# Performance work log

Hardware: AMD Instinct MI355X
Metric: run time of the kernel (lower is better)

Reference implementation:

```python
import jax, jax.numpy as jnp
import numpy as np

OUT_SIZE = 7          # output_size
RATIO = 2             # sampling_ratio
STRIDES = (4, 8, 16, 32)  # feature_map_strides, levels P2..P5
CANONICAL = 224.0


def _bilinear_sample(fm, ys, xs):
    """fm: [H,W,C]; ys: [R,K]; xs: [R,K] -> [R,K,K,C] samples at (y[r,ky], x[r,kx]).
    Out-of-range points (y<=-1 or y>=H, same for x) produce 0, matching ROIAlign."""
    H, W, C = fm.shape
    vy = (ys > -1.0) & (ys < H)
    vx = (xs > -1.0) & (xs < W)
    y = jnp.clip(ys, 0.0, H - 1.0)
    x = jnp.clip(xs, 0.0, W - 1.0)
    y0 = jnp.floor(y).astype(jnp.int32)
    x0 = jnp.floor(x).astype(jnp.int32)
    y1 = jnp.minimum(y0 + 1, H - 1)
    x1 = jnp.minimum(x0 + 1, W - 1)
    ly = y - y0; hy = 1.0 - ly  # [R,K]
    lx = x - x0; hx = 1.0 - lx
    f00 = fm[y0[:, :, None], x0[:, None, :]]  # [R,Ky,Kx,C]
    f01 = fm[y0[:, :, None], x1[:, None, :]]
    f10 = fm[y1[:, :, None], x0[:, None, :]]
    f11 = fm[y1[:, :, None], x1[:, None, :]]
    w00 = (hy[:, :, None] * hx[:, None, :])[..., None]
    w01 = (hy[:, :, None] * lx[:, None, :])[..., None]
    w10 = (ly[:, :, None] * hx[:, None, :])[..., None]
    w11 = (ly[:, :, None] * lx[:, None, :])[..., None]
    val = w00 * f00 + w01 * f01 + w10 * f10 + w11 * f11
    mask = (vy[:, :, None] & vx[:, None, :])[..., None]
    return jnp.where(mask, val, 0.0)


def _roi_align_one(fm, boxes):
    """fm: [H,W,C]; boxes: [R,4] in this feature map's coords -> [R,C,S,S]."""
    x1, y1, x2, y2 = boxes[:, 0], boxes[:, 1], boxes[:, 2], boxes[:, 3]
    rw = jnp.maximum(x2 - x1, 1.0)
    rh = jnp.maximum(y2 - y1, 1.0)
    S, r = OUT_SIZE, RATIO
    K = S * r
    g = (jnp.arange(K, dtype=jnp.float32) + 0.5) / r  # sample grid in bin units
    ys = y1[:, None] + g[None, :] * (rh / S)[:, None]  # [R,K]
    xs = x1[:, None] + g[None, :] * (rw / S)[:, None]
    v = _bilinear_sample(fm, ys, xs)                   # [R,K,K,C]
    R_ = v.shape[0]; C = fm.shape[-1]
    v = v.reshape(R_, S, r, S, r, C).mean(axis=(2, 4))  # avg over sampling points
    return v.transpose(0, 3, 1, 2)                      # [R,C,S,S]


def setup_inputs() -> dict:
    key = jax.random.key(0)
    ks = jax.random.split(key, 5)
    B, C, N = 4, 256, 512
    fm2 = jax.random.normal(ks[0], (B, 256, 256, C), dtype=jnp.float32)
    fm3 = jax.random.normal(ks[1], (B, 128, 128, C), dtype=jnp.float32)
    fm4 = jax.random.normal(ks[2], (B, 64, 64, C), dtype=jnp.float32)
    fm5 = jax.random.normal(ks[3], (B, 32, 32, C), dtype=jnp.float32)
    pts = jax.random.uniform(ks[4], (B, N, 2, 2), minval=0.0, maxval=1024.0)
    lo = jnp.min(pts, axis=2)  # [B,N,2] -> (x1,y1)
    hi = jnp.max(pts, axis=2)  # [B,N,2] -> (x2,y2)
    rois = jnp.concatenate([lo, hi], axis=-1)  # [B,N,4]
    return {"fm2": fm2, "fm3": fm3, "fm4": fm4, "fm5": fm5, "rois": rois}


def reference(fm2, fm3, fm4, fm5, rois):
    # FPN level assignment (image coords)
    x1, y1, x2, y2 = rois[..., 0], rois[..., 1], rois[..., 2], rois[..., 3]
    area = (y2 - y1) * (x2 - x1)
    lvl = jnp.log(jnp.sqrt(area) / CANONICAL) / jnp.log(2.0) + 4.0
    lvl = jnp.clip(jnp.round(lvl).astype(jnp.int32), 2, 5)  # [B,N]

    out = 0.0
    for i, (fm, stride) in enumerate(zip((fm2, fm3, fm4, fm5), STRIDES)):
        scale = 1.0 / stride
        aligned = jax.vmap(lambda f, b: _roi_align_one(f, b * scale))(fm, rois)
        out = out + jnp.where((lvl == i + 2)[:, :, None, None, None], aligned, 0.0)
    return out  # [B,N,C,S,S]
```

## Files before the change

kernel.cpp:

```cpp
#include <hip/hip_runtime.h>


constexpr int S     = 7;
constexpr int SS    = 49;
constexpr int CCH   = 256;
constexpr int NROI  = 512;
constexpr int BATCH = 4;
constexpr int CPAD  = 260;

__global__ __launch_bounds__(512, 4) void roialign_kernel(
    const float* __restrict__ fm2, const float* __restrict__ fm3,
    const float* __restrict__ fm4, const float* __restrict__ fm5,
    const float* __restrict__ rois, float* __restrict__ out)
{
    __shared__ float    tile[SS * CPAD];
    __shared__ float    s_wyh[14], s_wyl[14], s_wxh[14], s_wxl[14];
    __shared__ unsigned s_ry0[14], s_ry1[14], s_cx0[14], s_cx1[14];

    const int roi = blockIdx.x;
    const int b   = roi >> 9;

    const float x1  = rois[roi * 4 + 0];
    const float y1v = rois[roi * 4 + 1];
    const float x2  = rois[roi * 4 + 2];
    const float y2v = rois[roi * 4 + 3];

    const float area = (y2v - y1v) * (x2 - x1);
    const float lraw = logf(sqrtf(area) * (1.0f / 224.0f)) * 1.4426950408889634f + 4.0f;
    int lvl = (int)rintf(lraw);
    lvl = lvl < 2 ? 2 : (lvl > 5 ? 5 : lvl);

    const float* fm; int H; float scale;
    if (lvl == 2)      { fm = fm2; H = 256; scale = 0.25f;    }
    else if (lvl == 3) { fm = fm3; H = 128; scale = 0.125f;   }
    else if (lvl == 4) { fm = fm4; H = 64;  scale = 0.0625f;  }
    else               { fm = fm5; H = 32;  scale = 0.03125f; }
    const int W = H;
    fm += (size_t)b * H * W * CCH;

    const float bx1 = x1 * scale, by1 = y1v * scale;
    const float rw  = fmaxf(x2 * scale - bx1, 1.0f);
    const float rh  = fmaxf(y2v * scale - by1, 1.0f);
    const float stx = rw * (1.0f / 7.0f);
    const float sty = rh * (1.0f / 7.0f);

    const int t = threadIdx.x;

    if (t < 14) {
        const int k = t;
        const float yy = by1 + ((float)k + 0.5f) * 0.5f * sty;
        const float Hf = (float)H;
        const bool  v  = (yy > -1.0f) && (yy < Hf);
        const float yc = fminf(fmaxf(yy, 0.0f), Hf - 1.0f);
        const int   y0 = (int)floorf(yc);
        const int   y1i = min(y0 + 1, H - 1);
        const float ly = yc - (float)y0;
        s_wyl[k] = v ? ly : 0.0f;
        s_wyh[k] = v ? 1.0f - ly : 0.0f;
        s_ry0[k] = (unsigned)(y0  * W * (CCH * 4));
        s_ry1[k] = (unsigned)(y1i * W * (CCH * 4));
    } else if (t >= 64 && t < 78) {
        const int k = t - 64;
        const float xx = bx1 + ((float)k + 0.5f) * 0.5f * stx;
        const float Wf = (float)W;
        const bool  v  = (xx > -1.0f) && (xx < Wf);
        const float xc = fminf(fmaxf(xx, 0.0f), Wf - 1.0f);
        const int   x0 = (int)floorf(xc);
        const int   x1i = min(x0 + 1, W - 1);
        const float lx = xc - (float)x0;
        s_wxl[k] = v ? lx : 0.0f;
        s_wxh[k] = v ? 1.0f - lx : 0.0f;
        s_cx0[k] = (unsigned)(x0  * (CCH * 4));
        s_cx1[k] = (unsigned)(x1i * (CCH * 4));
    }
    __syncthreads();

    const int lane = t & 63;
    const int wv   = t >> 6;
    const unsigned cb = (unsigned)(lane << 4);

    const char* __restrict__ fmb = (const char*)fm;

    for (int bin = wv; bin < SS; bin += 8) {
        const int sy = bin / 7;
        const int sx = bin - sy * 7;
        const int ky = sy << 1, kx = sx << 1;

        const float hy0 = s_wyh[ky],     ly0 = s_wyl[ky];
        const float hy1 = s_wyh[ky + 1], ly1 = s_wyl[ky + 1];
        const float hx0 = s_wxh[kx],     lx0 = s_wxl[kx];
        const float hx1 = s_wxh[kx + 1], lx1 = s_wxl[kx + 1];
        const unsigned rA = s_ry0[ky],     rB = s_ry1[ky];
        const unsigned rC = s_ry0[ky + 1], rD = s_ry1[ky + 1];
        const unsigned cA = s_cx0[kx],     cB = s_cx1[kx];
        const unsigned cC = s_cx0[kx + 1], cD = s_cx1[kx + 1];

        float4 acc = make_float4(0.f, 0.f, 0.f, 0.f);

#define LD4(OFF) (*(const float4*)(fmb + (OFF)))
#define ACC4(Wt, F) \
        acc.x = fmaf((Wt), (F).x, acc.x); acc.y = fmaf((Wt), (F).y, acc.y); \
        acc.z = fmaf((Wt), (F).z, acc.z); acc.w = fmaf((Wt), (F).w, acc.w);

        const float4 fAA = LD4(rA + cA + cb);
        const float4 fAB = LD4(rA + cB + cb);
        const float4 fBA = LD4(rB + cA + cb);
        const float4 fBB = LD4(rB + cB + cb);
        const float4 fAC = LD4(rA + cC + cb);
        const float4 fAD = LD4(rA + cD + cb);
        const float4 fBC = LD4(rB + cC + cb);
        const float4 fBD = LD4(rB + cD + cb);
        const float4 fCA = LD4(rC + cA + cb);
        const float4 fCB = LD4(rC + cB + cb);
        const float4 fDA = LD4(rD + cA + cb);
        const float4 fDB = LD4(rD + cB + cb);
        const float4 fCC = LD4(rC + cC + cb);
        const float4 fCD = LD4(rC + cD + cb);
        const float4 fDC = LD4(rD + cC + cb);
        const float4 fDD = LD4(rD + cD + cb);

        ACC4(hy0 * hx0, fAA); ACC4(hy0 * lx0, fAB);
        ACC4(ly0 * hx0, fBA); ACC4(ly0 * lx0, fBB);
        ACC4(hy0 * hx1, fAC); ACC4(hy0 * lx1, fAD);
        ACC4(ly0 * hx1, fBC); ACC4(ly0 * lx1, fBD);
        ACC4(hy1 * hx0, fCA); ACC4(hy1 * lx0, fCB);
        ACC4(ly1 * hx0, fDA); ACC4(ly1 * lx0, fDB);
        ACC4(hy1 * hx1, fCC); ACC4(hy1 * lx1, fCD);
        ACC4(ly1 * hx1, fDC); ACC4(ly1 * lx1, fDD);
#undef LD4
#undef ACC4

        *(float4*)&tile[bin * CPAD + (lane << 2)] = make_float4(
            acc.x * 0.25f, acc.y * 0.25f, acc.z * 0.25f, acc.w * 0.25f);
    }

    __syncthreads();

    float* oreg = out + (size_t)roi * (CCH * SS);
    for (int i = t; i < (CCH * SS) / 4; i += 512) {
        const int f0 = i * 4;
        float4 v;
        { const int c = (f0 + 0) / SS, bn = (f0 + 0) - c * SS; v.x = tile[bn * CPAD + c]; }
        { const int c = (f0 + 1) / SS, bn = (f0 + 1) - c * SS; v.y = tile[bn * CPAD + c]; }
        { const int c = (f0 + 2) / SS, bn = (f0 + 2) - c * SS; v.z = tile[bn * CPAD + c]; }
        { const int c = (f0 + 3) / SS, bn = (f0 + 3) - c * SS; v.w = tile[bn * CPAD + c]; }
        *(float4*)(oreg + f0) = v;
    }
}

extern "C" void kernel_launch(void* const* d_in, const int* in_sizes, int n_in,
                              void* d_out, int out_size, void* d_ws, size_t ws_size,
                              hipStream_t stream) {
    const float* fm2  = (const float*)d_in[0];
    const float* fm3  = (const float*)d_in[1];
    const float* fm4  = (const float*)d_in[2];
    const float* fm5  = (const float*)d_in[3];
    const float* rois = (const float*)d_in[4];
    float* out = (float*)d_out;

    roialign_kernel<<<BATCH * NROI, 512, 0, stream>>>(fm2, fm3, fm4, fm5, rois, out);
}
```

Before: 75.67 us.

## Dedupe coincident bilinear taps, skip zero-weight loads, swizzle LDS tile

Merges the weights of bilinear taps that hit the same row or column, which happens when sampling points cluster at clamped edges or inside one pixel. Loads whose combined weight is zero are predicated off, cutting global memory traffic for small or out-of-bounds ROIs. The padded shared tile is replaced by an XOR-swizzled unpadded layout to avoid bank conflicts while using less LDS. The cost is extra per-bin compare and select logic and branches that may diverge.

```diff
diff --git a/kernel.cpp b/kernel.cpp
--- a/kernel.cpp
+++ b/kernel.cpp
@@ -6,14 +6,13 @@
 constexpr int CCH   = 256;
 constexpr int NROI  = 512;
 constexpr int BATCH = 4;
-constexpr int CPAD  = 260;
 
 __global__ __launch_bounds__(512, 4) void roialign_kernel(
     const float* __restrict__ fm2, const float* __restrict__ fm3,
     const float* __restrict__ fm4, const float* __restrict__ fm5,
     const float* __restrict__ rois, float* __restrict__ out)
 {
-    __shared__ float    tile[SS * CPAD];
+    __shared__ float    tile[SS * CCH];
     __shared__ float    s_wyh[14], s_wyl[14], s_wxh[14], s_wxl[14];
     __shared__ unsigned s_ry0[14], s_ry1[14], s_cx0[14], s_cx1[14];
 
@@ -80,58 +79,84 @@
     const unsigned cb = (unsigned)(lane << 4);
 
     const char* __restrict__ fmb = (const char*)fm;
+    const float4 z4 = make_float4(0.f, 0.f, 0.f, 0.f);
 
     for (int bin = wv; bin < SS; bin += 8) {
         const int sy = bin / 7;
         const int sx = bin - sy * 7;
         const int ky = sy << 1, kx = sx << 1;
 
-        const float hy0 = s_wyh[ky],     ly0 = s_wyl[ky];
-        const float hy1 = s_wyh[ky + 1], ly1 = s_wyl[ky + 1];
-        const float hx0 = s_wxh[kx],     lx0 = s_wxl[kx];
-        const float hx1 = s_wxh[kx + 1], lx1 = s_wxl[kx + 1];
-        const unsigned rA = s_ry0[ky],     rB = s_ry1[ky];
+        float w0 = s_wyh[ky], w1 = s_wyl[ky], w2 = s_wyh[ky + 1], w3 = s_wyl[ky + 1];
+        const unsigned rA = s_ry0[ky], rB = s_ry1[ky];
         const unsigned rC = s_ry0[ky + 1], rD = s_ry1[ky + 1];
-        const unsigned cA = s_cx0[kx],     cB = s_cx1[kx];
+        {
+            const bool eBA = (rB == rA);
+            w0 += eBA ? w1 : 0.f;  w1 = eBA ? 0.f : w1;
+            const bool eCA = (rC == rA);
+            const bool eCB = !eCA && (rC == rB);
+            w0 += eCA ? w2 : 0.f;  w1 += eCB ? w2 : 0.f;
+            w2 = (eCA || eCB) ? 0.f : w2;
+            const bool eDA = (rD == rA);
+            const bool eDB = !eDA && (rD == rB);
+            const bool eDC = !eDA && !eDB && (rD == rC);
+            w0 += eDA ? w3 : 0.f;  w1 += eDB ? w3 : 0.f;  w2 += eDC ? w3 : 0.f;
+            w3 = (eDA || eDB || eDC) ? 0.f : w3;
+        }
+        float u0 = s_wxh[kx], u1 = s_wxl[kx], u2 = s_wxh[kx + 1], u3 = s_wxl[kx + 1];
+        const unsigned cA = s_cx0[kx], cB = s_cx1[kx];
         const unsigned cC = s_cx0[kx + 1], cD = s_cx1[kx + 1];
-
-        float4 acc = make_float4(0.f, 0.f, 0.f, 0.f);
+        {
+            const bool eBA = (cB == cA);
+            u0 += eBA ? u1 : 0.f;  u1 = eBA ? 0.f : u1;
+            const bool eCA = (cC == cA);
+            const bool eCB = !eCA && (cC == cB);
+            u0 += eCA ? u2 : 0.f;  u1 += eCB ? u2 : 0.f;
+            u2 = (eCA || eCB) ? 0.f : u2;
+            const bool eDA = (cD == cA);
+            const bool eDB = !eDA && (cD == cB);
+            const bool eDC = !eDA && !eDB && (cD == cC);
+            u0 += eDA ? u3 : 0.f;  u1 += eDB ? u3 : 0.f;  u2 += eDC ? u3 : 0.f;
+            u3 = (eDA || eDB || eDC) ? 0.f : u3;
+        }
+
+        const bool gr0 = (w0 != 0.f), gr1 = (w1 != 0.f);
+        const bool gr2 = (w2 != 0.f), gr3 = (w3 != 0.f);
+        const bool gc0 = (u0 != 0.f), gc1 = (u1 != 0.f);
+        const bool gc2 = (u2 != 0.f), gc3 = (u3 != 0.f);
 
 #define LD4(OFF) (*(const float4*)(fmb + (OFF)))
-#define ACC4(Wt, F) \
-        acc.x = fmaf((Wt), (F).x, acc.x); acc.y = fmaf((Wt), (F).y, acc.y); \
-        acc.z = fmaf((Wt), (F).z, acc.z); acc.w = fmaf((Wt), (F).w, acc.w);
-
-        const float4 fAA = LD4(rA + cA + cb);
-        const float4 fAB = LD4(rA + cB + cb);
-        const float4 fBA = LD4(rB + cA + cb);
-        const float4 fBB = LD4(rB + cB + cb);
-        const float4 fAC = LD4(rA + cC + cb);
-        const float4 fAD = LD4(rA + cD + cb);
-        const float4 fBC = LD4(rB + cC + cb);
-        const float4 fBD = LD4(rB + cD + cb);
-        const float4 fCA = LD4(rC + cA + cb);
-        const float4 fCB = LD4(rC + cB + cb);
-        const float4 fDA = LD4(rD + cA + cb);
-        const float4 fDB = LD4(rD + cB + cb);
-        const float4 fCC = LD4(rC + cC + cb);
-        const float4 fCD = LD4(rC + cD + cb);
-        const float4 fDC = LD4(rD + cC + cb);
-        const float4 fDD = LD4(rD + cD + cb);
-
-        ACC4(hy0 * hx0, fAA); ACC4(hy0 * lx0, fAB);
-        ACC4(ly0 * hx0, fBA); ACC4(ly0 * lx0, fBB);
-        ACC4(hy0 * hx1, fAC); ACC4(hy0 * lx1, fAD);
-        ACC4(ly0 * hx1, fBC); ACC4(ly0 * lx1, fBD);
-        ACC4(hy1 * hx0, fCA); ACC4(hy1 * lx0, fCB);
-        ACC4(ly1 * hx0, fDA); ACC4(ly1 * lx0, fDB);
-        ACC4(hy1 * hx1, fCC); ACC4(hy1 * lx1, fCD);
-        ACC4(ly1 * hx1, fDC); ACC4(ly1 * lx1, fDD);
+        const float4 f00 = (gr0 && gc0) ? LD4(rA + cA + cb) : z4;
+        const float4 f01 = (gr0 && gc1) ? LD4(rA + cB + cb) : z4;
+        const float4 f02 = (gr0 && gc2) ? LD4(rA + cC + cb) : z4;
+        const float4 f03 = (gr0 && gc3) ? LD4(rA + cD + cb) : z4;
+        const float4 f10 = (gr1 && gc0) ? LD4(rB + cA + cb) : z4;
+        const float4 f11 = (gr1 && gc1) ? LD4(rB + cB + cb) : z4;
+        const float4 f12 = (gr1 && gc2) ? LD4(rB + cC + cb) : z4;
+        const float4 f13 = (gr1 && gc3) ? LD4(rB + cD + cb) : z4;
+        const float4 f20 = (gr2 && gc0) ? LD4(rC + cA + cb) : z4;
+        const float4 f21 = (gr2 && gc1) ? LD4(rC + cB + cb) : z4;
+        const float4 f22 = (gr2 && gc2) ? LD4(rC + cC + cb) : z4;
+        const float4 f23 = (gr2 && gc3) ? LD4(rC + cD + cb) : z4;
+        const float4 f30 = (gr3 && gc0) ? LD4(rD + cA + cb) : z4;
+        const float4 f31 = (gr3 && gc1) ? LD4(rD + cB + cb) : z4;
+        const float4 f32 = (gr3 && gc2) ? LD4(rD + cC + cb) : z4;
+        const float4 f33 = (gr3 && gc3) ? LD4(rD + cD + cb) : z4;
 #undef LD4
+
+        float4 acc = z4;
+#define ACC4(Wt, F) { const float pw_ = (Wt); \
+        acc.x = fmaf(pw_, (F).x, acc.x); acc.y = fmaf(pw_, (F).y, acc.y); \
+        acc.z = fmaf(pw_, (F).z, acc.z); acc.w = fmaf(pw_, (F).w, acc.w); }
+        ACC4(w0 * u0, f00); ACC4(w0 * u1, f01); ACC4(w0 * u2, f02); ACC4(w0 * u3, f03);
+        ACC4(w1 * u0, f10); ACC4(w1 * u1, f11); ACC4(w1 * u2, f12); ACC4(w1 * u3, f13);
+        ACC4(w2 * u0, f20); ACC4(w2 * u1, f21); ACC4(w2 * u2, f22); ACC4(w2 * u3, f23);
+        ACC4(w3 * u0, f30); ACC4(w3 * u1, f31); ACC4(w3 * u2, f32); ACC4(w3 * u3, f33);
 #undef ACC4
 
-        *(float4*)&tile[bin * CPAD + (lane << 2)] = make_float4(
-            acc.x * 0.25f, acc.y * 0.25f, acc.z * 0.25f, acc.w * 0.25f);
+        const unsigned xsw = (((unsigned)bin >> 2) & 7u) << 2;
+        float* dst = &tile[bin * CCH + ((unsigned)(lane << 2) ^ xsw)];
+        *(float4*)dst = make_float4(acc.x * 0.25f, acc.y * 0.25f,
+                                    acc.z * 0.25f, acc.w * 0.25f);
     }
 
     __syncthreads();
@@ -140,10 +165,26 @@
     for (int i = t; i < (CCH * SS) / 4; i += 512) {
         const int f0 = i * 4;
         float4 v;
-        { const int c = (f0 + 0) / SS, bn = (f0 + 0) - c * SS; v.x = tile[bn * CPAD + c]; }
-        { const int c = (f0 + 1) / SS, bn = (f0 + 1) - c * SS; v.y = tile[bn * CPAD + c]; }
-        { const int c = (f0 + 2) / SS, bn = (f0 + 2) - c * SS; v.z = tile[bn * CPAD + c]; }
-        { const int c = (f0 + 3) / SS, bn = (f0 + 3) - c * SS; v.w = tile[bn * CPAD + c]; }
+        {
+            const int f = f0 + 0;
+            const int c = f / SS, bn = f - c * SS;
+            v.x = tile[bn * CCH + (c ^ ((((unsigned)bn >> 2) & 7u) << 2))];
+        }
+        {
+            const int f = f0 + 1;
+            const int c = f / SS, bn = f - c * SS;
+            v.y = tile[bn * CCH + (c ^ ((((unsigned)bn >> 2) & 7u) << 2))];
+        }
+        {
+            const int f = f0 + 2;
+            const int c = f / SS, bn = f - c * SS;
+            v.z = tile[bn * CCH + (c ^ ((((unsigned)bn >> 2) & 7u) << 2))];
+        }
+        {
+            const int f = f0 + 3;
+            const int c = f / SS, bn = f - c * SS;
+            v.w = tile[bn * CCH + (c ^ ((((unsigned)bn >> 2) & 7u) << 2))];
+        }
         *(float4*)(oreg + f0) = v;
     }
 }
```

Result: slower. 242.2 us (+220.1%).
